# Kernel optimization log

Measured on AMD Instinct MI355X. Metric: run time of the kernel, lower is better.

## Reference

```python
import jax, jax.numpy as jnp
import numpy as np

N_LAYER = 2


def setup_inputs() -> dict:
    key = jax.random.key(0)
    k1, k2 = jax.random.split(key)
    seq_len, batch, hidden = 2048, 32, 512
    x = jax.random.normal(k1, (seq_len, batch, hidden), dtype=jnp.float32)
    # torch init: uniform(0, 1) on recurrent weights
    w_hh = jax.random.uniform(k2, (N_LAYER, hidden), dtype=jnp.float32)
    h0 = jnp.zeros((N_LAYER, batch, hidden), dtype=jnp.float32)
    return {"x": x, "w_hh": w_hh, "h0": h0}


def reference(x, w_hh, h0):
    # x: [T, B, H]; w_hh: [L, H]; h0: [L, B, H]
    out = x
    for i in range(N_LAYER):
        w = w_hh[i]  # [H]

        def step(h, xt):
            h_new = jax.nn.relu(xt + h * w)
            return h_new, h_new

        _, out = jax.lax.scan(step, h0[i], out)  # out: [T, B, H]
    return out
```

## Files before the change

### kernel.cpp

```cpp
#include <hip/hip_runtime.h>


#define TSTEPS 2048
#define BATCH  32
#define HID    512
#define BH     (BATCH * HID)
#define U      16
#define D      4
#define NBLK   (TSTEPS / U)

__global__ __launch_bounds__(64, 1) void indrnn_fused_kernel(
    const float* __restrict__ x,
    const float* __restrict__ w_hh,
    const float* __restrict__ h0,
    float* __restrict__ out) {
  const int c   = blockIdx.x * 64 + threadIdx.x;
  const int hid = c & (HID - 1);

  const float w1 = w_hh[hid];
  const float w2 = w_hh[HID + hid];
  float h1 = h0[c];
  float h2 = h0[BH + c];

  const float* xp = x + c;
  float*       op = out + c;

  float buf[D][U];

#pragma unroll
  for (int d = 0; d < D - 1; ++d) {
    const float* xn = xp + (size_t)d * U * BH;
#pragma unroll
    for (int u = 0; u < U; ++u)
      buf[d][u] = xn[(size_t)u * BH];
  }

  for (int blk0 = 0; blk0 < NBLK; blk0 += D) {
#pragma unroll
    for (int d = 0; d < D; ++d) {
      const int blk  = blk0 + d;
      const int pblk = blk + (D - 1);
      if (pblk < NBLK) {
        const float* xn = xp + (size_t)pblk * U * BH;
#pragma unroll
        for (int u = 0; u < U; ++u)
          buf[(d + D - 1) & (D - 1)][u] = xn[(size_t)u * BH];
      }
      float* ob = op + (size_t)blk * U * BH;
#pragma unroll
      for (int u = 0; u < U; ++u) {
        h1 = fmaxf(fmaf(w1, h1, buf[d][u]), 0.0f);
        h2 = fmaxf(fmaf(w2, h2, h1), 0.0f);
        ob[(size_t)u * BH] = h2;
      }
    }
  }
}

extern "C" void kernel_launch(void* const* d_in, const int* in_sizes, int n_in,
                              void* d_out, int out_size, void* d_ws, size_t ws_size,
                              hipStream_t stream) {
  const float* x    = (const float*)d_in[0];
  const float* w_hh = (const float*)d_in[1];
  const float* h0   = (const float*)d_in[2];
  float* out        = (float*)d_out;

  dim3 grid(BH / 64);
  dim3 block(64);
  hipLaunchKernelGGL(indrnn_fused_kernel, grid, block, 0, stream,
                     x, w_hh, h0, out);
}
```

Measured before the change: 243.5 us.

## Parallelize IndRNN recurrence over time with chunked max-affine scan

Splits the 2048-step sequence into 32 chunks, each handled by its own group of 32 threads. Each chunk's ReLU recurrence is summarised as a function of the form max(w^64·h + a, b). A single thread then scans these summaries serially to get each chunk's starting hidden state, done once per layer, and a final pass recomputes both layers and writes the output. This trades the serial 2048-step latency chain for far more parallelism, at the cost of reading x three times instead of once. The summary composition is exact only when the recurrent weights are nonnegative.

```diff
diff --git a/kernel.cpp b/kernel.cpp
--- a/kernel.cpp
+++ b/kernel.cpp
@@ -5,55 +5,86 @@
 #define BATCH  32
 #define HID    512
 #define BH     (BATCH * HID)
-#define U      16
-#define D      4
-#define NBLK   (TSTEPS / U)
+#define CH     32
+#define NC     32
+#define CL     (TSTEPS / NC)
 
-__global__ __launch_bounds__(64, 1) void indrnn_fused_kernel(
+__global__ __launch_bounds__(1024, 8) void indrnn_scan_kernel(
     const float* __restrict__ x,
     const float* __restrict__ w_hh,
     const float* __restrict__ h0,
     float* __restrict__ out) {
-  const int c   = blockIdx.x * 64 + threadIdx.x;
+  const int tid = threadIdx.x;
+  const int chl = tid & (CH - 1);
+  const int ci  = tid >> 5;
+  const int c   = blockIdx.x * CH + chl;
   const int hid = c & (HID - 1);
 
   const float w1 = w_hh[hid];
   const float w2 = w_hh[HID + hid];
-  float h1 = h0[c];
-  float h2 = h0[BH + c];
+  float s1 = w1, s2 = w2;
+#pragma unroll
+  for (int i = 0; i < 6; ++i) { s1 *= s1; s2 *= s2; }
 
-  const float* xp = x + c;
-  float*       op = out + c;
+  __shared__ float A[NC][CH], B[NC][CH], HS1[NC][CH], HS2[NC][CH];
 
-  float buf[D][U];
+  const size_t base = (size_t)ci * CL * BH + c;
+  const float* xp = x + base;
+  float*       op = out + base;
 
+  float a1 = 0.f, b1 = 0.f;
+#pragma unroll 4
+  for (int s = 0; s < CL; ++s) {
+    float xv = xp[(size_t)s * BH];
+    a1 = fmaf(w1, a1, xv);
+    b1 = fmaxf(fmaf(w1, b1, xv), 0.f);
+  }
+  A[ci][chl] = a1;
+  B[ci][chl] = b1;
+  __syncthreads();
+
+  if (ci == 0) {
+    float h = h0[c];
 #pragma unroll
-  for (int d = 0; d < D - 1; ++d) {
-    const float* xn = xp + (size_t)d * U * BH;
+    for (int k = 0; k < NC; ++k) {
+      HS1[k][chl] = h;
+      h = fmaxf(fmaf(s1, h, A[k][chl]), B[k][chl]);
+    }
+  }
+  __syncthreads();
+
+  float h1 = HS1[ci][chl];
+  float a2 = 0.f, b2 = 0.f;
+#pragma unroll 4
+  for (int s = 0; s < CL; ++s) {
+    float xv = xp[(size_t)s * BH];
+    h1 = fmaxf(fmaf(w1, h1, xv), 0.f);
+    a2 = fmaf(w2, a2, h1);
+    b2 = fmaxf(fmaf(w2, b2, h1), 0.f);
+  }
+  __syncthreads();
+  A[ci][chl] = a2;
+  B[ci][chl] = b2;
+  __syncthreads();
+
+  if (ci == 0) {
+    float h = h0[BH + c];
 #pragma unroll
-    for (int u = 0; u < U; ++u)
-      buf[d][u] = xn[(size_t)u * BH];
+    for (int k = 0; k < NC; ++k) {
+      HS2[k][chl] = h;
+      h = fmaxf(fmaf(s2, h, A[k][chl]), B[k][chl]);
+    }
   }
+  __syncthreads();
 
-  for (int blk0 = 0; blk0 < NBLK; blk0 += D) {
-#pragma unroll
-    for (int d = 0; d < D; ++d) {
-      const int blk  = blk0 + d;
-      const int pblk = blk + (D - 1);
-      if (pblk < NBLK) {
-        const float* xn = xp + (size_t)pblk * U * BH;
-#pragma unroll
-        for (int u = 0; u < U; ++u)
-          buf[(d + D - 1) & (D - 1)][u] = xn[(size_t)u * BH];
-      }
-      float* ob = op + (size_t)blk * U * BH;
-#pragma unroll
-      for (int u = 0; u < U; ++u) {
-        h1 = fmaxf(fmaf(w1, h1, buf[d][u]), 0.0f);
-        h2 = fmaxf(fmaf(w2, h2, h1), 0.0f);
-        ob[(size_t)u * BH] = h2;
-      }
-    }
+  h1 = HS1[ci][chl];
+  float h2 = HS2[ci][chl];
+#pragma unroll 4
+  for (int s = 0; s < CL; ++s) {
+    float xv = xp[(size_t)s * BH];
+    h1 = fmaxf(fmaf(w1, h1, xv), 0.f);
+    h2 = fmaxf(fmaf(w2, h2, h1), 0.f);
+    op[(size_t)s * BH] = h2;
   }
 }
 
@@ -65,8 +96,8 @@
   const float* h0   = (const float*)d_in[2];
   float* out        = (float*)d_out;
 
-  dim3 grid(BH / 64);
-  dim3 block(64);
-  hipLaunchKernelGGL(indrnn_fused_kernel, grid, block, 0, stream,
+  dim3 grid(BH / CH);
+  dim3 block(CH * NC);
+  hipLaunchKernelGGL(indrnn_scan_kernel, grid, block, 0, stream,
                      x, w_hh, h0, out);
 }
```

After: 284.0 us. +16.6%, slower.
